# Performance work log

Hardware: AMD Instinct MI355X
Metric: run time of the kernel (lower is better)

Reference implementation:

```python
import jax, jax.numpy as jnp
import numpy as np
from jax import lax

EPS = 1e-10

def _ln(x, g, b):
    m = x.mean(-1, keepdims=True)
    v = x.var(-1, keepdims=True)
    return (x - m) / jnp.sqrt(v + 1e-5) * g + b

def _gather(t, idx):
    # t: (B, HW, c), idx: (B, HW, d) -> (B, HW, d, c); out[n,i,k,:] = t[n, idx[n,i,k], :]
    return jax.vmap(lambda tn, In: tn[In])(t, idx)

def setup_inputs() -> dict:
    key = jax.random.key(0)
    ks = jax.random.split(key, 20)
    b, v, c, d, h, w, hid, ksz = 2, 2, 128, 64, 64, 64, 256, 5
    hw = h * w
    Bf = b * v  # v_1 == 1 target view per reference view
    std = 0.02
    return {
        'features_mv': jax.random.normal(ks[0], (b, v, c, h, w), jnp.float32),
        'warp_indices': jax.random.randint(ks[1], (Bf, hw, d), 0, hw, jnp.int32),
        'depth_prob': jax.random.uniform(ks[2], (Bf, hw, d), jnp.float32),
        'ln1_g': jnp.ones((c,), jnp.float32), 'ln1_b': jnp.zeros((c,), jnp.float32),
        'wq': jax.random.normal(ks[3], (c, c), jnp.float32) * std, 'bq': jnp.zeros((c,), jnp.float32),
        'wk': jax.random.normal(ks[4], (c, c), jnp.float32) * std, 'bk': jnp.zeros((c,), jnp.float32),
        'wv': jax.random.normal(ks[5], (c, c), jnp.float32) * std, 'bv': jnp.zeros((c,), jnp.float32),
        'k_pe': jax.random.normal(ks[6], (1, 1, d), jnp.float32) * std,
        'v_pe': jax.random.normal(ks[7], (1, 1, d), jnp.float32) * std,
        'rpe': jax.random.normal(ks[8], (1, 1, d), jnp.float32) * std,
        'proj_w': jax.random.normal(ks[9], (c, c), jnp.float32) * std, 'proj_b': jnp.zeros((c,), jnp.float32),
        'ln2_g': jnp.ones((c,), jnp.float32), 'ln2_b': jnp.zeros((c,), jnp.float32),
        'fc1_w': jax.random.normal(ks[10], (c, hid), jnp.float32) * std, 'fc1_b': jnp.zeros((hid,), jnp.float32),
        'dw_w': jax.random.normal(ks[11], (hid, 1, ksz, ksz), jnp.float32) * std, 'dw_b': jnp.zeros((hid,), jnp.float32),
        'fc2_w': jax.random.normal(ks[12], (hid, c), jnp.float32) * std, 'fc2_b': jnp.zeros((c,), jnp.float32),
    }

def reference(features_mv, warp_indices, depth_prob, ln1_g, ln1_b, wq, bq, wk, bk, wv, bv,
              k_pe, v_pe, rpe, proj_w, proj_b, ln2_g, ln2_b, fc1_w, fc1_b, dw_w, dw_b, fc2_w, fc2_b):
    b, v, c, h, w = features_mv.shape
    hw = h * w
    hid = fc1_w.shape[1]
    scale = c ** (-0.5)  # num_heads = 1 -> head_dim = dim

    # (b v) (h w) c
    x = features_mv.reshape(b * v, c, hw).transpose(0, 2, 1)
    shortcut = x
    xn = _ln(x, ln1_g, ln1_b)
    q = xn @ wq + bq
    k = xn @ wk + bk
    vv = xn @ wv + bv

    # nn pairing: v=2, v_1=1 -> each reference view attends the other view
    Q = (q.reshape(b, v, hw, c) * scale).reshape(b * v, hw, c)
    K = k.reshape(b, v, hw, c)[:, ::-1].reshape(b * v, hw, c)
    V = vv.reshape(b, v, hw, c)[:, ::-1].reshape(b * v, hw, c)

    # SMM_QmK: cost[n,i,k] = sum_c Q[n,i,c] * K[n, idx[n,i,k], c]
    Kg = _gather(K, warp_indices)                       # (B, hw, d, c)
    cost = jnp.einsum('bic,bikc->bik', Q, Kg)
    Q_pe = Q.sum(-1, keepdims=True)                     # (B, hw, 1)
    cost = cost + Q_pe * k_pe + rpe                     # broadcast (1,1,d)

    # (Sim_UNet similarity refinement omitted: UNetModel source unavailable; identity here)
    attn = jax.nn.softmax(cost, axis=-1)
    attn = attn * depth_prob
    attn = (attn + EPS) / (attn.sum(-1, keepdims=True) + EPS)

    # SMM_AmV: out[n,i,c] = sum_k attn[n,i,k] * V[n, idx[n,i,k], c]
    Vg = _gather(V, warp_indices)                       # (B, hw, d, c)
    out = jnp.einsum('bik,bikc->bic', attn, Vg)
    out = out + (attn * v_pe).sum(-1, keepdims=True)

    # projection + residual (v_1 == 1 so B == b*v)
    x = shortcut + (out @ proj_w + proj_b)

    # ConvFFN residual branch
    xn2 = _ln(x, ln2_g, ln2_b)
    y = jax.nn.gelu(xn2 @ fc1_w + fc1_b, approximate=False)
    yi = y.transpose(0, 2, 1).reshape(b * v, hid, h, w)
    yc = lax.conv_general_dilated(yi, dw_w, (1, 1), 'SAME', feature_group_count=hid,
                                  dimension_numbers=('NCHW', 'OIHW', 'NCHW'))
    yc = jax.nn.gelu(yc + dw_b[None, :, None, None], approximate=False)
    y = y + yc.reshape(b * v, hid, hw).transpose(0, 2, 1)
    y = y @ fc2_w + fc2_b
    return x + y
```

## Files before the change

kernel.cpp:

```cpp
#include <hip/hip_runtime.h>
#include <math.h>

#define TOK   16384
#define HW    4096
#define C     128
#define D     64
#define HID   256

constexpr float LN_EPS = 1e-5f;
constexpr float EPS_R  = 1e-10f;
constexpr float QSCALE = 0.08838834764831845f;

typedef __attribute__((ext_vector_type(8))) short  bf16x8;
typedef __attribute__((ext_vector_type(4))) float  f32x4;
typedef __attribute__((ext_vector_type(2))) _Float16 half2v;
#define MFMA16(a, b, c) __builtin_amdgcn_mfma_f32_16x16x32_bf16((a), (b), (c), 0, 0, 0)
#define SBAR() __builtin_amdgcn_sched_barrier(0)

__device__ __forceinline__ float bflo(unsigned u) { return __uint_as_float(u << 16); }
__device__ __forceinline__ float bfhi(unsigned u) { return __uint_as_float(u & 0xffff0000u); }
__device__ __forceinline__ unsigned short f2bf(float f) {
  unsigned u = __float_as_uint(f);
  unsigned r = (u + 0x7fffu + ((u >> 16) & 1u)) >> 16;
  return (unsigned short)r;
}
__device__ __forceinline__ unsigned short f2h(float f) {
  _Float16 h = (_Float16)f;
  unsigned short r;
  __builtin_memcpy(&r, &h, 2);
  return r;
}
__device__ __forceinline__ float gelu_exact(float x) {
  return 0.5f * x * (1.0f + erff(x * 0.7071067811865476f));
}

union U4H { uint4 v; half2v h[4]; };
union U1H { unsigned v; half2v h; };

#if __has_builtin(__builtin_amdgcn_fdot2)
__device__ __forceinline__ float dot2h(half2v a, half2v b, float c) {
  return __builtin_amdgcn_fdot2(a, b, c, false);
}
#else
__device__ __forceinline__ float dot2h(half2v a, half2v b, float c) {
  return c + (float)a.x * (float)b.x + (float)a.y * (float)b.y;
}
#endif

__global__ __launch_bounds__(256) void k_prep(const float* __restrict__ wq,
    const float* __restrict__ wk, const float* __restrict__ wv,
    const float* __restrict__ pw, const float* __restrict__ f1w,
    const float* __restrict__ f2w, unsigned short* __restrict__ wt) {
  int id = blockIdx.x * 256 + threadIdx.x;
  if (id < 16384) {
    int n = id >> 7, k = id & 127;
    wt[id] = f2bf(wq[k * 128 + n]);
  } else if (id < 32768) {
    int e = id - 16384; int n = e >> 7, k = e & 127;
    wt[id] = f2bf(wk[k * 128 + n]);
  } else if (id < 49152) {
    int e = id - 32768; int n = e >> 7, k = e & 127;
    wt[id] = f2bf(wv[k * 128 + n]);
  } else if (id < 65536) {
    int e = id - 49152; int n = e >> 7, k = e & 127;
    wt[id] = f2bf(pw[k * 128 + n]);
  } else if (id < 98304) {
    int e = id - 65536; int n = e >> 7, k = e & 127;
    wt[id] = f2bf(f1w[k * 256 + n]);
  } else {
    int e = id - 98304; int n = e >> 8, k = e & 255;
    wt[id] = f2bf(f2w[k * 128 + n]);
  }
}

__global__ __launch_bounds__(256) void k_ln1qkv(const float* __restrict__ feat,
    const float* __restrict__ g, const float* __restrict__ b,
    const unsigned short* __restrict__ wt,
    const float* __restrict__ bq, const float* __restrict__ bk,
    const float* __restrict__ bv, unsigned short* __restrict__ qh,
    unsigned short* __restrict__ ksw, unsigned short* __restrict__ vsw) {
  __shared__ float t16[16][C + 1];
  __shared__ unsigned short axn[16 * C];
  int tid = threadIdx.x;
  int lane = tid & 63, wave = tid >> 6;
  int t0 = blockIdx.x * 16;
  int nv = t0 >> 12, i0 = t0 & 4095;
  const float* fb = feat + (size_t)nv * C * HW;
  for (int e = tid; e < 16 * C; e += 256) {
    int ch = e >> 4, ii = e & 15;
    t16[ii][ch] = fb[(size_t)ch * HW + i0 + ii];
  }
  __syncthreads();
  for (int tkn = wave; tkn < 16; tkn += 4) {
    float a0 = t16[tkn][lane];
    float a1 = t16[tkn][lane + 64];
    float s = a0 + a1;
    for (int off = 32; off; off >>= 1) s += __shfl_xor(s, off, 64);
    float mean = s * (1.0f / 128.0f);
    float d0 = a0 - mean, d1 = a1 - mean;
    float v = d0 * d0 + d1 * d1;
    for (int off = 32; off; off >>= 1) v += __shfl_xor(v, off, 64);
    float rstd = rsqrtf(v * (1.0f / 128.0f) + LN_EPS);
    unsigned short x0 = f2bf(d0 * rstd * g[lane] + b[lane]);
    unsigned short x1 = f2bf(d1 * rstd * g[lane + 64] + b[lane + 64]);
    int b0 = (tkn * 256 + lane * 2) ^ ((tkn & 15) << 4);
    int b1 = (tkn * 256 + (lane + 64) * 2) ^ ((tkn & 15) << 4);
    *(unsigned short*)((char*)axn + b0) = x0;
    *(unsigned short*)((char*)axn + b1) = x1;
  }
  __syncthreads();
  int q4 = lane >> 4, m = lane & 15;
  bf16x8 a[4];
  #pragma unroll
  for (int ks = 0; ks < 4; ks++) {
    int boff = (m * 256 + ks * 64 + q4 * 16) ^ (m << 4);
    a[ks] = *(const bf16x8*)((char*)axn + boff);
  }
  int swbase = ((nv ^ 1) << 12) + i0;
  #pragma unroll
  for (int tt = 0; tt < 6; ++tt) {
    int gt = wave * 6 + tt;
    int mat = gt >> 3, ct = gt & 7;
    const unsigned short* bp = wt + mat * 16384 + (size_t)(ct * 16 + m) * C + q4 * 8;
    f32x4 acc = (f32x4){0.f, 0.f, 0.f, 0.f};
    #pragma unroll
    for (int ks = 0; ks < 4; ks++) {
      bf16x8 bfrag = *(const bf16x8*)(bp + ks * 32);
      acc = MFMA16(a[ks], bfrag, acc);
    }
    const float* B = (mat == 0) ? bq : ((mat == 1) ? bk : bv);
    float sc = (mat == 0) ? QSCALE : 1.0f;
    unsigned short* O = (mat == 0) ? qh : ((mat == 1) ? ksw : vsw);
    int base = (mat == 0) ? t0 : swbase;
    int col = ct * 16 + m;
    float bb = B[col];
    #pragma unroll
    for (int reg = 0; reg < 4; reg++) {
      int row = base + q4 * 4 + reg;
      O[(size_t)row * C + col] = f2h((acc[reg] + bb) * sc);
    }
  }
}

__global__ __launch_bounds__(256, 4) void k_attn_proj_fc1(
    const unsigned short* __restrict__ qh, const unsigned short* __restrict__ ksw,
    const unsigned short* __restrict__ vsw, const int* __restrict__ widx,
    const float* __restrict__ dprob, const float* __restrict__ kpe,
    const float* __restrict__ vpe, const float* __restrict__ rpe,
    const unsigned short* __restrict__ wt, const float* __restrict__ pb,
    const float* __restrict__ feat, float* __restrict__ xio,
    const float* __restrict__ g2, const float* __restrict__ b2,
    const float* __restrict__ f1b, unsigned short* __restrict__ y) {
  __shared__ unsigned short axn[16 * C];
  __shared__ float ps1[4][16];
  __shared__ float ps2[4][16];
  int lane = threadIdx.x & 63;
  int wave = threadIdx.x >> 6;
  int bid = blockIdx.x;
  int n = (bid >> 1) & 3;
  int within = ((bid >> 3) << 1) | (bid & 1);
  int T0 = n * HW + within * 16;
  const unsigned short* Kb = ksw + (size_t)n * HW * C;
  const unsigned short* Vb = vsw + (size_t)n * HW * C;
  int gg = lane >> 3, s = lane & 7;
  half2v ones = {(_Float16)1.0f, (_Float16)1.0f};
  float kpe_l = kpe[lane], rpe_l = rpe[lane], vpe_l = vpe[lane];
  float Svpe = vpe_l;
  for (int off = 32; off; off >>= 1) Svpe += __shfl_xor(Svpe, off, 64);

  for (int tj = 0; tj < 4; ++tj) {
    int token = T0 + wave * 4 + tj;
    int myidx = widx[(size_t)token * D + lane];
    float mydp = dprob[(size_t)token * D + lane];
    half2v qreg[8];
    {
      const unsigned short* qp = qh + (size_t)token * C + s * 16;
      U4H qa, qb2;
      qa.v = *(const uint4*)(qp);
      qb2.v = *(const uint4*)(qp + 8);
      #pragma unroll
      for (int i = 0; i < 4; i++) { qreg[i] = qa.h[i]; qreg[4 + i] = qb2.h[i]; }
    }
    int rowv[8];
    #pragma unroll
    for (int pass = 0; pass < 8; ++pass)
      rowv[pass] = __shfl(myidx, pass * 8 + gg, 64);
    uint4 ka[8], kb[8];
    #pragma unroll
    for (int pass = 0; pass < 8; ++pass) {
      const unsigned short* kr = Kb + (size_t)rowv[pass] * C + s * 16;
      ka[pass] = *(const uint4*)(kr);
      kb[pass] = *(const uint4*)(kr + 8);
    }
    unsigned vv0[32];
    #pragma unroll
    for (int j = 0; j < 32; j++) {
      int row = __builtin_amdgcn_readlane(myidx, j);
      vv0[j] = *(const unsigned*)(Vb + (size_t)row * C + lane * 2);
    }
    SBAR();
    float qpe = 0.f;
    #pragma unroll
    for (int i = 0; i < 8; i++) qpe = dot2h(qreg[i], ones, qpe);
    qpe += __shfl_xor(qpe, 1, 64);
    qpe += __shfl_xor(qpe, 2, 64);
    qpe += __shfl_xor(qpe, 4, 64);
    float mycost = 0.f;
    #pragma unroll
    for (int pass = 0; pass < 8; ++pass) {
      U4H ua, ub;
      ua.v = ka[pass]; ub.v = kb[pass];
      float p = 0.f;
      #pragma unroll
      for (int i = 0; i < 4; i++) p = dot2h(ua.h[i], qreg[i], p);
      #pragma unroll
      for (int i = 0; i < 4; i++) p = dot2h(ub.h[i], qreg[4 + i], p);
      p += __shfl_xor(p, 1, 64);
      p += __shfl_xor(p, 2, 64);
      p += __shfl_xor(p, 4, 64);
      float t = __shfl(p, (lane & 7) << 3, 64);
      if (pass == gg) mycost = t;
    }
    mycost += qpe * kpe_l + rpe_l;
    SBAR();
    unsigned vv1[32];
    #pragma unroll
    for (int j = 0; j < 32; j++) {
      int row = __builtin_amdgcn_readlane(myidx, 32 + j);
      vv1[j] = *(const unsigned*)(Vb + (size_t)row * C + lane * 2);
    }
    SBAR();
    float mx = mycost;
    for (int off = 32; off; off >>= 1) mx = fmaxf(mx, __shfl_xor(mx, off, 64));
    float e = __expf(mycost - mx);
    float e1 = e * mydp;
    float e2 = e1 * vpe_l;
    float S0 = e, S1 = e1, S2 = e2;
    for (int off = 32; off; off >>= 1) {
      S0 += __shfl_xor(S0, off, 64);
      S1 += __shfl_xor(S1, off, 64);
      S2 += __shfl_xor(S2, off, 64);
    }
    float r = 1.0f / (S1 + EPS_R * S0);
    float attn = (e1 + EPS_R * S0) * r;
    float vpt = (S2 + EPS_R * S0 * Svpe) * r;
    SBAR();
    float o0 = vpt, o1 = vpt;
    unsigned att_u = __float_as_uint(attn);
    #pragma unroll
    for (int j = 0; j < 32; j++) {
      float a = __uint_as_float(__builtin_amdgcn_readlane(att_u, j));
      U1H h; h.v = vv0[j];
      o0 += a * (float)h.h.x;
      o1 += a * (float)h.h.y;
    }
    #pragma unroll
    for (int j = 0; j < 32; j++) {
      float a = __uint_as_float(__builtin_amdgcn_readlane(att_u, 32 + j));
      U1H h; h.v = vv1[j];
      o0 += a * (float)h.h.x;
      o1 += a * (float)h.h.y;
    }
    unsigned pk = (unsigned)f2bf(o0) | ((unsigned)f2bf(o1) << 16);
    int row = wave * 4 + tj;
    int boff = (row * 256 + lane * 4) ^ ((row & 15) << 4);
    *(unsigned*)((char*)axn + boff) = pk;
  }
  __syncthreads();

  int q4 = lane >> 4, m = lane & 15;
  bf16x8 a[4];
  #pragma unroll
  for (int ks = 0; ks < 4; ks++) {
    int boff = (m * 256 + ks * 64 + q4 * 16) ^ (m << 4);
    a[ks] = *(const bf16x8*)((char*)axn + boff);
  }
  const unsigned short* Wp = wt + 3 * 16384;
  f32x4 acc[2];
  #pragma unroll
  for (int nt = 0; nt < 2; nt++) acc[nt] = (f32x4){0.f, 0.f, 0.f, 0.f};
  #pragma unroll
  for (int nt = 0; nt < 2; nt++) {
    int colt = wave * 32 + nt * 16;
    const unsigned short* bp = Wp + (size_t)(colt + m) * C + q4 * 8;
    #pragma unroll
    for (int ks = 0; ks < 4; ks++) {
      bf16x8 bfrag = *(const bf16x8*)(bp + ks * 32);
      acc[nt] = MFMA16(a[ks], bfrag, acc[nt]);
    }
  }
  int ibase = (T0 & 4095) + q4 * 4;
  float s1[4] = {0.f, 0.f, 0.f, 0.f}, s2b[4] = {0.f, 0.f, 0.f, 0.f};
  #pragma unroll
  for (int nt = 0; nt < 2; nt++) {
    int col = wave * 32 + nt * 16 + m;
    float bb = pb[col];
    const float* fp = feat + ((size_t)n * C + col) * HW + ibase;
    #pragma unroll
    for (int reg = 0; reg < 4; reg++) {
      float v = acc[nt][reg] + bb + fp[reg];
      acc[nt][reg] = v;
      s1[reg] += v;
      s2b[reg] += v * v;
    }
  }
  #pragma unroll
  for (int reg = 0; reg < 4; reg++) {
    #pragma unroll
    for (int off = 1; off < 16; off <<= 1) {
      s1[reg] += __shfl_xor(s1[reg], off, 64);
      s2b[reg] += __shfl_xor(s2b[reg], off, 64);
    }
  }
  if (m == 0) {
    #pragma unroll
    for (int reg = 0; reg < 4; reg++) {
      ps1[wave][q4 * 4 + reg] = s1[reg];
      ps2[wave][q4 * 4 + reg] = s2b[reg];
    }
  }
  __syncthreads();
  float mean[4], rstd[4];
  #pragma unroll
  for (int reg = 0; reg < 4; reg++) {
    int row = q4 * 4 + reg;
    float t1 = ps1[0][row] + ps1[1][row] + ps1[2][row] + ps1[3][row];
    float t2 = ps2[0][row] + ps2[1][row] + ps2[2][row] + ps2[3][row];
    mean[reg] = t1 * (1.0f / 128.0f);
    float var = t2 * (1.0f / 128.0f) - mean[reg] * mean[reg];
    rstd[reg] = rsqrtf(var + LN_EPS);
  }
  #pragma unroll
  for (int nt = 0; nt < 2; nt++) {
    int col = wave * 32 + nt * 16 + m;
    float gc = g2[col], bc = b2[col];
    #pragma unroll
    for (int reg = 0; reg < 4; reg++) {
      int row = q4 * 4 + reg;
      float v = acc[nt][reg];
      xio[(size_t)(T0 + row) * C + col] = v;
      unsigned short xv = f2bf((v - mean[reg]) * rstd[reg] * gc + bc);
      int boff = (row * 256 + col * 2) ^ ((row & 15) << 4);
      *(unsigned short*)((char*)axn + boff) = xv;
    }
  }
  __syncthreads();

  bf16x8 af[4];
  #pragma unroll
  for (int ks = 0; ks < 4; ks++) {
    int boff = (m * 256 + ks * 64 + q4 * 16) ^ (m << 4);
    af[ks] = *(const bf16x8*)((char*)axn + boff);
  }
  const unsigned short* Wf = wt + 65536;
  #pragma unroll
  for (int nt = 0; nt < 4; nt++) {
    int colt = wave * 64 + nt * 16;
    const unsigned short* bp = Wf + (size_t)(colt + m) * C + q4 * 8;
    f32x4 acc2 = (f32x4){0.f, 0.f, 0.f, 0.f};
    #pragma unroll
    for (int ks = 0; ks < 4; ks++) {
      bf16x8 bfrag = *(const bf16x8*)(bp + ks * 32);
      acc2 = MFMA16(af[ks], bfrag, acc2);
    }
    int col = colt + m;
    float bb = f1b[col];
    #pragma unroll
    for (int reg = 0; reg < 4; reg++) {
      int row = T0 + q4 * 4 + reg;
      y[(size_t)row * HID + col] = f2bf(gelu_exact(acc2[reg] + bb));
    }
  }
}

__global__ __launch_bounds__(256) void k_dwconv(const unsigned short* __restrict__ y,
    const float* __restrict__ w, const float* __restrict__ bias,
    unsigned short* __restrict__ ysum) {
  __shared__ float tile[8][401];
  __shared__ float wl[8][25];
  __shared__ float bl[8];
  __shared__ unsigned short outl[256][8];
  int bid = blockIdx.x;
  int tile_id = bid & 15;
  int cb = (bid >> 4) & 31;
  int n = bid >> 9;
  int ty = (tile_id >> 2) * 16, tx = (tile_id & 3) * 16;
  int ch0 = cb * 8;
  int tid = threadIdx.x;
  if (tid < 200) wl[tid / 25][tid % 25] = w[(size_t)(ch0 + tid / 25) * 25 + tid % 25];
  if (tid < 8) bl[tid] = bias[ch0 + tid];
  const unsigned short* yb = y + (size_t)n * HW * HID;
  for (int p = tid; p < 400; p += 256) {
    int py = p / 20, px = p % 20;
    int gy = ty + py - 2, gx = tx + px - 2;
    uint4 v = make_uint4(0u, 0u, 0u, 0u);
    if (gy >= 0 && gy < 64 && gx >= 0 && gx < 64)
      v = *(const uint4*)(yb + (size_t)(gy * 64 + gx) * HID + ch0);
    tile[0][p] = bflo(v.x); tile[1][p] = bfhi(v.x);
    tile[2][p] = bflo(v.y); tile[3][p] = bfhi(v.y);
    tile[4][p] = bflo(v.z); tile[5][p] = bfhi(v.z);
    tile[6][p] = bflo(v.w); tile[7][p] = bfhi(v.w);
  }
  __syncthreads();
  int cc = tid & 7;
  int xx = (tid >> 3) & 15;
  int yg = tid >> 7;
  float wreg[25];
  #pragma unroll
  for (int k = 0; k < 25; k++) wreg[k] = wl[cc][k];
  float bb = bl[cc];
  float win[12][5];
  #pragma unroll
  for (int r = 0; r < 12; r++)
    #pragma unroll
    for (int dx = 0; dx < 5; dx++)
      win[r][dx] = tile[cc][(yg * 8 + r) * 20 + xx + dx];
  #pragma unroll
  for (int j = 0; j < 8; ++j) {
    float acc = 0.f;
    #pragma unroll
    for (int dy = 0; dy < 5; ++dy)
      #pragma unroll
      for (int dx = 0; dx < 5; ++dx)
        acc += wreg[dy * 5 + dx] * win[j + dy][dx];
    float o = win[j + 2][2] + gelu_exact(acc + bb);
    int yy = yg * 8 + j;
    outl[yy * 16 + xx][cc] = f2bf(o);
  }
  __syncthreads();
  {
    int p = tid;
    int yy = p >> 4, xx2 = p & 15;
    uint4 val = *(const uint4*)outl[p];
    *(uint4*)(ysum + (size_t)(n * HW + (ty + yy) * 64 + tx + xx2) * HID + ch0) = val;
  }
}

__global__ __launch_bounds__(256) void k_fc2(const unsigned short* __restrict__ ysum,
    const unsigned short* __restrict__ wt, const float* __restrict__ f2b,
    const float* __restrict__ xio, float* __restrict__ outp) {
  int w = threadIdx.x >> 6, lane = threadIdx.x & 63;
  int q4 = lane >> 4, m = lane & 15;
  int t0 = blockIdx.x * 64 + w * 16;
  int quarter = blockIdx.y;
  const unsigned short* Wt = wt + 98304;
  const unsigned short* ap = ysum + (size_t)(t0 + m) * HID + q4 * 8;
  bf16x8 a[8];
  #pragma unroll
  for (int ks = 0; ks < 8; ks++) a[ks] = *(const bf16x8*)(ap + ks * 32);
  f32x4 acc[2];
  #pragma unroll
  for (int nt = 0; nt < 2; nt++) acc[nt] = (f32x4){0.f, 0.f, 0.f, 0.f};
  #pragma unroll
  for (int nt = 0; nt < 2; nt++) {
    const unsigned short* bp = Wt + (size_t)(quarter * 32 + nt * 16 + m) * HID + q4 * 8;
    #pragma unroll
    for (int ks = 0; ks < 8; ks++) {
      bf16x8 bfrag = *(const bf16x8*)(bp + ks * 32);
      acc[nt] = MFMA16(a[ks], bfrag, acc[nt]);
    }
  }
  #pragma unroll
  for (int nt = 0; nt < 2; nt++) {
    int col = quarter * 32 + nt * 16 + m;
    float bb = f2b[col];
    #pragma unroll
    for (int reg = 0; reg < 4; reg++) {
      int row = t0 + q4 * 4 + reg;
      outp[(size_t)row * C + col] = acc[nt][reg] + bb + xio[(size_t)row * C + col];
    }
  }
}

extern "C" void kernel_launch(void* const* d_in, const int* in_sizes, int n_in,
                              void* d_out, int out_size, void* d_ws, size_t ws_size,
                              hipStream_t stream) {
  (void)in_sizes; (void)n_in; (void)out_size; (void)ws_size;
  const float* feat  = (const float*)d_in[0];
  const int*   widx  = (const int*)d_in[1];
  const float* dprob = (const float*)d_in[2];
  const float* ln1g  = (const float*)d_in[3];
  const float* ln1b  = (const float*)d_in[4];
  const float* wq    = (const float*)d_in[5];
  const float* bq    = (const float*)d_in[6];
  const float* wk    = (const float*)d_in[7];
  const float* bk    = (const float*)d_in[8];
  const float* wv    = (const float*)d_in[9];
  const float* bv    = (const float*)d_in[10];
  const float* kpe   = (const float*)d_in[11];
  const float* vpe   = (const float*)d_in[12];
  const float* rpe   = (const float*)d_in[13];
  const float* pw    = (const float*)d_in[14];
  const float* pb    = (const float*)d_in[15];
  const float* ln2g  = (const float*)d_in[16];
  const float* ln2b  = (const float*)d_in[17];
  const float* f1w   = (const float*)d_in[18];
  const float* f1b   = (const float*)d_in[19];
  const float* dww   = (const float*)d_in[20];
  const float* dwb   = (const float*)d_in[21];
  const float* f2w   = (const float*)d_in[22];
  const float* f2b   = (const float*)d_in[23];

  float* ws = (float*)d_ws;
  const size_t M2 = (size_t)TOK * C;
  float* xio = ws;
  unsigned short* qhb   = (unsigned short*)(ws + M2);
  unsigned short* ksb   = (unsigned short*)(ws + 2 * M2);
  unsigned short* vsb   = (unsigned short*)(ws + 2 * M2 + M2 / 2);
  unsigned short* yb    = (unsigned short*)(ws + 3 * M2);
  unsigned short* ysumb = (unsigned short*)(ws + 4 * M2);
  unsigned short* wtb   = (unsigned short*)(ws + 5 * M2);

  k_prep   <<<512, 256, 0, stream>>>(wq, wk, wv, pw, f1w, f2w, wtb);
  k_ln1qkv <<<1024, 256, 0, stream>>>(feat, ln1g, ln1b, wtb, bq, bk, bv, qhb, ksb, vsb);
  k_attn_proj_fc1<<<1024, 256, 0, stream>>>(qhb, ksb, vsb, widx, dprob, kpe, vpe,
                                            rpe, wtb, pb, feat, xio, ln2g, ln2b,
                                            f1b, yb);
  k_dwconv <<<2048, 256, 0, stream>>>(yb, dww, dwb, ysumb);
  k_fc2    <<<dim3(TOK / 64, 4), 256, 0, stream>>>(ysumb, wtb, f2b, xio, (float*)d_out);
}
```

Before: 199.8 us.

## Stage gathered V rows into LDS via global_load_lds instead of registers

The V-row gather in the attention kernel now issues all 64 row loads per token directly into a per-wave 16 KB LDS buffer using global_load_lds, rather than holding 64 values in VGPRs across two phases. This lowers register pressure and lets every gather be in flight while the cost and softmax are computed. The price is 64 KB of shared memory per block, which caps occupancy at a couple of blocks per CU, and the launch-bounds occupancy hint is dropped. The attention outputs are kept in registers until a barrier, after which the shared buffer is reused for the projection/LN staging.

```diff
diff --git a/kernel.cpp b/kernel.cpp
--- a/kernel.cpp
+++ b/kernel.cpp
@@ -15,7 +15,6 @@
 typedef __attribute__((ext_vector_type(4))) float  f32x4;
 typedef __attribute__((ext_vector_type(2))) _Float16 half2v;
 #define MFMA16(a, b, c) __builtin_amdgcn_mfma_f32_16x16x32_bf16((a), (b), (c), 0, 0, 0)
-#define SBAR() __builtin_amdgcn_sched_barrier(0)
 
 __device__ __forceinline__ float bflo(unsigned u) { return __uint_as_float(u << 16); }
 __device__ __forceinline__ float bfhi(unsigned u) { return __uint_as_float(u & 0xffff0000u); }
@@ -46,6 +45,12 @@
   return c + (float)a.x * (float)b.x + (float)a.y * (float)b.y;
 }
 #endif
+
+__device__ __forceinline__ void gload_lds4(const void* g, void* l) {
+  __builtin_amdgcn_global_load_lds(
+      (const __attribute__((address_space(1))) void*)g,
+      (__attribute__((address_space(3))) void*)l, 4, 0, 0);
+}
 
 __global__ __launch_bounds__(256) void k_prep(const float* __restrict__ wq,
     const float* __restrict__ wk, const float* __restrict__ wv,
@@ -142,7 +147,7 @@
   }
 }
 
-__global__ __launch_bounds__(256, 4) void k_attn_proj_fc1(
+__global__ __launch_bounds__(256) void k_attn_proj_fc1(
     const unsigned short* __restrict__ qh, const unsigned short* __restrict__ ksw,
     const unsigned short* __restrict__ vsw, const int* __restrict__ widx,
     const float* __restrict__ dprob, const float* __restrict__ kpe,
@@ -151,9 +156,7 @@
     const float* __restrict__ feat, float* __restrict__ xio,
     const float* __restrict__ g2, const float* __restrict__ b2,
     const float* __restrict__ f1b, unsigned short* __restrict__ y) {
-  __shared__ unsigned short axn[16 * C];
-  __shared__ float ps1[4][16];
-  __shared__ float ps2[4][16];
+  __shared__ __align__(16) char smem[65536];
   int lane = threadIdx.x & 63;
   int wave = threadIdx.x >> 6;
   int bid = blockIdx.x;
@@ -161,13 +164,15 @@
   int within = ((bid >> 3) << 1) | (bid & 1);
   int T0 = n * HW + within * 16;
   const unsigned short* Kb = ksw + (size_t)n * HW * C;
-  const unsigned short* Vb = vsw + (size_t)n * HW * C;
+  const unsigned* Vb_u = (const unsigned*)(vsw + (size_t)n * HW * C);
+  unsigned* vwp = (unsigned*)smem + wave * 4096;
   int gg = lane >> 3, s = lane & 7;
   half2v ones = {(_Float16)1.0f, (_Float16)1.0f};
   float kpe_l = kpe[lane], rpe_l = rpe[lane], vpe_l = vpe[lane];
   float Svpe = vpe_l;
   for (int off = 32; off; off >>= 1) Svpe += __shfl_xor(Svpe, off, 64);
 
+  unsigned pks[4];
   for (int tj = 0; tj < 4; ++tj) {
     int token = T0 + wave * 4 + tj;
     int myidx = widx[(size_t)token * D + lane];
@@ -192,13 +197,13 @@
       ka[pass] = *(const uint4*)(kr);
       kb[pass] = *(const uint4*)(kr + 8);
     }
-    unsigned vv0[32];
-    #pragma unroll
-    for (int j = 0; j < 32; j++) {
+    asm volatile("s_waitcnt lgkmcnt(0)" ::: "memory");
+    #pragma unroll
+    for (int j = 0; j < 64; j++) {
       int row = __builtin_amdgcn_readlane(myidx, j);
-      vv0[j] = *(const unsigned*)(Vb + (size_t)row * C + lane * 2);
-    }
-    SBAR();
+      gload_lds4(Vb_u + (size_t)row * 64 + lane, vwp + j * 64);
+    }
+    asm volatile("" ::: "memory");
     float qpe = 0.f;
     #pragma unroll
     for (int i = 0; i < 8; i++) qpe = dot2h(qreg[i], ones, qpe);
@@ -222,14 +227,6 @@
       if (pass == gg) mycost = t;
     }
     mycost += qpe * kpe_l + rpe_l;
-    SBAR();
-    unsigned vv1[32];
-    #pragma unroll
-    for (int j = 0; j < 32; j++) {
-      int row = __builtin_amdgcn_readlane(myidx, 32 + j);
-      vv1[j] = *(const unsigned*)(Vb + (size_t)row * C + lane * 2);
-    }
-    SBAR();
     float mx = mycost;
     for (int off = 32; off; off >>= 1) mx = fmaxf(mx, __shfl_xor(mx, off, 64));
     float e = __expf(mycost - mx);
@@ -244,27 +241,28 @@
     float r = 1.0f / (S1 + EPS_R * S0);
     float attn = (e1 + EPS_R * S0) * r;
     float vpt = (S2 + EPS_R * S0 * Svpe) * r;
-    SBAR();
+    asm volatile("s_waitcnt vmcnt(0)" ::: "memory");
     float o0 = vpt, o1 = vpt;
     unsigned att_u = __float_as_uint(attn);
     #pragma unroll
-    for (int j = 0; j < 32; j++) {
+    for (int j = 0; j < 64; j++) {
       float a = __uint_as_float(__builtin_amdgcn_readlane(att_u, j));
-      U1H h; h.v = vv0[j];
+      U1H h; h.v = vwp[j * 64 + lane];
       o0 += a * (float)h.h.x;
       o1 += a * (float)h.h.y;
     }
-    #pragma unroll
-    for (int j = 0; j < 32; j++) {
-      float a = __uint_as_float(__builtin_amdgcn_readlane(att_u, 32 + j));
-      U1H h; h.v = vv1[j];
-      o0 += a * (float)h.h.x;
-      o1 += a * (float)h.h.y;
-    }
-    unsigned pk = (unsigned)f2bf(o0) | ((unsigned)f2bf(o1) << 16);
+    pks[tj] = (unsigned)f2bf(o0) | ((unsigned)f2bf(o1) << 16);
+  }
+  __syncthreads();
+
+  unsigned short* axn = (unsigned short*)smem;
+  float* ps1 = (float*)(smem + 4096);
+  float* ps2 = (float*)(smem + 4352);
+  #pragma unroll
+  for (int tj = 0; tj < 4; ++tj) {
     int row = wave * 4 + tj;
     int boff = (row * 256 + lane * 4) ^ ((row & 15) << 4);
-    *(unsigned*)((char*)axn + boff) = pk;
+    *(unsigned*)((char*)axn + boff) = pks[tj];
   }
   __syncthreads();
 
@@ -315,8 +313,8 @@
   if (m == 0) {
     #pragma unroll
     for (int reg = 0; reg < 4; reg++) {
-      ps1[wave][q4 * 4 + reg] = s1[reg];
-      ps2[wave][q4 * 4 + reg] = s2b[reg];
+      ps1[wave * 16 + q4 * 4 + reg] = s1[reg];
+      ps2[wave * 16 + q4 * 4 + reg] = s2b[reg];
     }
   }
   __syncthreads();
@@ -324,8 +322,8 @@
   #pragma unroll
   for (int reg = 0; reg < 4; reg++) {
     int row = q4 * 4 + reg;
-    float t1 = ps1[0][row] + ps1[1][row] + ps1[2][row] + ps1[3][row];
-    float t2 = ps2[0][row] + ps2[1][row] + ps2[2][row] + ps2[3][row];
+    float t1 = ps1[row] + ps1[16 + row] + ps1[32 + row] + ps1[48 + row];
+    float t2 = ps2[row] + ps2[16 + row] + ps2[32 + row] + ps2[48 + row];
     mean[reg] = t1 * (1.0f / 128.0f);
     float var = t2 * (1.0f / 128.0f) - mean[reg] * mean[reg];
     rstd[reg] = rsqrtf(var + LN_EPS);
```

After: 237.0 us. 18.6% more time.
